# Optimization experiments

Measured on AMD Instinct MI355X. Metric: run time of the kernel, lower is better.

Reference implementation:

```python
import jax, jax.numpy as jnp
import numpy as np

DIM = 1024
CTX_DIM = 768
H = 16


def setup_inputs() -> dict:
    key = jax.random.key(0)
    k1, k2, k3, k4, k5 = jax.random.split(key, 5)
    x = jax.random.normal(k1, (2, 2048, DIM), dtype=jnp.float32)
    context = jax.random.normal(k2, (2, 2048, CTX_DIM), dtype=jnp.float32)
    # Linear weights stored as [in, out] (y = x @ W); no biases per module.
    s = 0.02
    Wq = jax.random.normal(k3, (DIM, DIM), dtype=jnp.float32) * s
    Wkv = jax.random.normal(k4, (CTX_DIM, 2 * DIM), dtype=jnp.float32) * s
    Wo = jax.random.normal(k5, (DIM, DIM), dtype=jnp.float32) * s
    return {"x": x, "context": context, "Wq": Wq, "Wkv": Wkv, "Wo": Wo}


def reference(x, context, Wq, Wkv, Wo):
    B, N, C = x.shape
    Dh = C // H  # head dim
    scale = Dh ** -0.5
    M = context.shape[1]
    q = (x @ Wq).reshape(B, N, H, Dh).transpose(0, 2, 1, 3)      # [B,H,N,Dh]
    kv = context @ Wkv                                            # [B,M,2C]
    k, v = jnp.split(kv, 2, axis=-1)
    k = k.reshape(B, M, H, Dh).transpose(0, 2, 1, 3)              # [B,H,M,Dh]
    v = v.reshape(B, M, H, Dh).transpose(0, 2, 1, 3)              # [B,H,M,Dh]
    attn = jax.nn.softmax(jnp.einsum('bhnd,bhmd->bhnm', q, k) * scale, axis=-1)
    out = jnp.einsum('bhnm,bhmd->bhnd', attn, v)                  # [B,H,N,Dh]
    out = out.transpose(0, 2, 1, 3).reshape(B, N, C)
    return out @ Wo  # dropout is identity in eval / p=0
```

## Files before the change

### kernel.cpp

```cpp
#include <hip/hip_runtime.h>

typedef __attribute__((ext_vector_type(4))) float f32x4;
typedef __attribute__((ext_vector_type(8))) short short8;
typedef __attribute__((ext_vector_type(4))) unsigned int u32x4;
typedef unsigned short u16;
typedef unsigned int u32;
typedef unsigned long long u64;

__device__ __forceinline__ u16 f2bf(float f) {
  u32 u = __builtin_bit_cast(u32, f);
  u += 0x7fffu + ((u >> 16) & 1u);
  return (u16)(u >> 16);
}
__device__ __forceinline__ u16 f2bf_t(float f) {
  return (u16)(__builtin_bit_cast(u32, f) >> 16);
}

__device__ __forceinline__ void gl2lds16(const u16* g, const u16* l) {
  __builtin_amdgcn_global_load_lds(
      (const __attribute__((address_space(1))) u32*)g,
      (__attribute__((address_space(3))) u32*)(u32)(u64)l,
      16, 0, 0);
}

__device__ __forceinline__ void cast_body(const float* __restrict__ s,
                                          u16* __restrict__ d, int blk,
                                          int tid) {
  long i = (long)blk * 256 + tid;
  const f32x4* sp = (const f32x4*)(s + i * 8);
  f32x4 a = sp[0], b = sp[1];
  u16 t[8];
#pragma unroll
  for (int j = 0; j < 4; j++) {
    t[j] = f2bf(a[j]);
    t[4 + j] = f2bf(b[j]);
  }
  *(u32x4*)(d + i * 8) = *(u32x4*)t;
}

__device__ __forceinline__ void transpose_body(const float* __restrict__ W,
                                               u16* __restrict__ WT, int K,
                                               int N, int k0, int n0, int tid,
                                               u16* T) {
#pragma unroll
  for (int i = 0; i < 4; i++) {
    int c = tid + 256 * i;
    int row = c >> 4;
    int ch = c & 15;
    f32x4 f = *(const f32x4*)(W + (long)(k0 + row) * N + n0 + ch * 4);
#pragma unroll
    for (int j = 0; j < 4; j++) T[(ch * 4 + j) * 72 + row] = f2bf(f[j]);
  }
  __syncthreads();
#pragma unroll
  for (int i = 0; i < 2; i++) {
    int c = tid + 256 * i;
    int row = c >> 3;
    int ch = c & 7;
    u32x4 v = *(u32x4*)&T[row * 72 + ch * 8];
    *(u32x4*)(WT + (long)(n0 + row) * K + k0 + ch * 8) = v;
  }
}

__global__ __launch_bounds__(256) void prep(
    const float* __restrict__ x, const float* __restrict__ ctx,
    const float* __restrict__ Wq, const float* __restrict__ Wkv,
    const float* __restrict__ Wo, u16* __restrict__ xb,
    u16* __restrict__ ctxb, u16* __restrict__ wqT, u16* __restrict__ wkvT,
    u16* __restrict__ woT) {
  __shared__ __align__(16) u16 T[64 * 72];
  const int b = blockIdx.x, tid = threadIdx.x;
  if (b < 2048) {
    cast_body(x, xb, b, tid);
  } else if (b < 3584) {
    cast_body(ctx, ctxb, b - 2048, tid);
  } else if (b < 3840) {
    int idx = b - 3584;
    transpose_body(Wq, wqT, 1024, 1024, (idx >> 4) * 64, (idx & 15) * 64, tid, T);
  } else if (b < 4224) {
    int idx = b - 3840;
    transpose_body(Wkv, wkvT, 768, 2048, (idx >> 5) * 64, (idx & 31) * 64, tid, T);
  } else {
    int idx = b - 4224;
    transpose_body(Wo, woT, 1024, 1024, (idx >> 4) * 64, (idx & 15) * 64, tid, T);
  }
}

__device__ __forceinline__ void gemm128_core(
    const u16* __restrict__ A, const u16* __restrict__ Bt, int Kstride,
    int Klen, long brow, long bcol, int tid, u16* As, u16* Bs,
    f32x4 (&acc)[4][4]) {
  const int lane = tid & 63, wv = tid >> 6;
  const int l15 = lane & 15, quad = lane >> 4;
  const int wr = (wv >> 1) * 64, wc = (wv & 1) * 64;
  const int sr = lane >> 3, sc = lane & 7;
  const int csw = ((sc ^ sr) & 7) * 8;

  const u16* ag[4];
  const u16* bg[4];
  const u16* al[4];
  const u16* bl[4];
#pragma unroll
  for (int n = 0; n < 4; n++) {
    int row = wv * 32 + n * 8;
    ag[n] = A + (brow + row + sr) * (long)Kstride + csw;
    al[n] = &As[row * 64];
    bg[n] = Bt + (bcol + row + sr) * (long)Kstride + csw;
    bl[n] = &Bs[row * 64];
  }

  for (int kt = 0; kt < Klen; kt += 64) {
    __syncthreads();
#pragma unroll
    for (int n = 0; n < 4; n++) gl2lds16(ag[n] + kt, al[n]);
#pragma unroll
    for (int n = 0; n < 4; n++) gl2lds16(bg[n] + kt, bl[n]);
    __syncthreads();
#pragma unroll
    for (int kk = 0; kk < 2; kk++) {
      short8 af[4], bf[4];
#pragma unroll
      for (int i = 0; i < 4; i++) {
        int row = wr + i * 16 + l15;
        af[i] = *(short8*)&As[row * 64 + (((kk * 4 + quad) ^ (row & 7)) << 3)];
      }
#pragma unroll
      for (int j = 0; j < 4; j++) {
        int row = wc + j * 16 + l15;
        bf[j] = *(short8*)&Bs[row * 64 + (((kk * 4 + quad) ^ (row & 7)) << 3)];
      }
#pragma unroll
      for (int i = 0; i < 4; i++)
#pragma unroll
        for (int j = 0; j < 4; j++)
          acc[i][j] = __builtin_amdgcn_mfma_f32_16x16x32_bf16(
              af[i], bf[j], acc[i][j], 0, 0, 0);
    }
  }
}

__global__ __launch_bounds__(256, 3) void fused_qkv(
    const u16* __restrict__ xb, const u16* __restrict__ ctxb,
    const u16* __restrict__ wqT, const u16* __restrict__ wkvT,
    u16* __restrict__ Qb, u16* __restrict__ Kfrag, u16* __restrict__ Vfrag,
    float qscale) {
  __shared__ __align__(16) u16 As[128 * 64];
  __shared__ __align__(16) u16 Bs[128 * 64];
  const int tid = threadIdx.x;
  const int lane = tid & 63, wv = tid >> 6;
  const int l15 = lane & 15, quad = lane >> 4;
  const int wr = (wv >> 1) * 64, wc = (wv & 1) * 64;

  f32x4 acc[4][4];
#pragma unroll
  for (int i = 0; i < 4; i++)
#pragma unroll
    for (int j = 0; j < 4; j++) acc[i][j] = (f32x4){0.f, 0.f, 0.f, 0.f};

  int bid = blockIdx.x;
  if (bid < 256) {
    long brow = (long)(bid >> 3) * 128, bcol = (long)(bid & 7) * 128;
    gemm128_core(xb, wqT, 1024, 1024, brow, bcol, tid, As, Bs, acc);
#pragma unroll
    for (int i = 0; i < 4; i++)
#pragma unroll
      for (int j = 0; j < 4; j++)
#pragma unroll
        for (int r = 0; r < 4; r++) {
          long row = brow + wr + i * 16 + quad * 4 + r;
          long col = bcol + wc + j * 16 + l15;
          Qb[row * 1024 + col] = f2bf(acc[i][j][r] * qscale);
        }
    return;
  }

  bid -= 256;
  long brow = (long)(bid >> 4) * 128, bcol = (long)(bid & 15) * 128;
  gemm128_core(ctxb, wkvT, 768, 768, brow, bcol, tid, As, Bs, acc);

  const bool is_k = (bcol < 1024);
  __syncthreads();
#pragma unroll
  for (int round = 0; round < 2; round++) {
    if ((wv >> 1) == round) {
      if (is_k) {
#pragma unroll
        for (int i = 0; i < 4; i++)
#pragma unroll
          for (int j = 0; j < 4; j++) {
            int d = j * 16 + l15;
            int off = (wv & 1) * 4096 + ((d >> 5) * 4 + i) * 512 +
                      (((d >> 3) & 3) * 16 + quad * 4) * 8 + (d & 7);
#pragma unroll
            for (int r = 0; r < 4; r++) As[off + r * 8] = f2bf(acc[i][j][r]);
          }
      } else {
#pragma unroll
        for (int i = 0; i < 4; i++)
#pragma unroll
          for (int j = 0; j < 4; j++) {
            int off = (wv & 1) * 4096 + ((i >> 1) * 4 + j) * 512 +
                      (quad * 16 + l15) * 8 + (i & 1) * 4;
            u16 t4[4];
#pragma unroll
            for (int r = 0; r < 4; r++) t4[r] = f2bf(acc[i][j][r]);
            *(u64*)&As[off] = *(const u64*)t4;
          }
      }
    }
    __syncthreads();
    long mg = brow + round * 64;
    int b_ = (int)(mg >> 11), mt = (int)((mg >> 6) & 31);
#pragma unroll
    for (int h2 = 0; h2 < 2; h2++) {
      int h = (int)((is_k ? bcol : bcol - 1024) >> 6) + h2;
      u16* dst = (is_k ? Kfrag : Vfrag) + ((long)(b_ * 16 + h) * 32 + mt) * 4096;
#pragma unroll
      for (int p = 0; p < 2; p++) {
        int c = p * 256 + tid;
        *(u32x4*)(dst + c * 8) = *(u32x4*)&As[h2 * 4096 + c * 8];
      }
    }
    __syncthreads();
  }
}

__global__ __launch_bounds__(256, 3) void gemm_o(
    const u16* __restrict__ A, const u16* __restrict__ Bt,
    float* __restrict__ C) {
  __shared__ __align__(16) u16 As[128 * 64];
  __shared__ __align__(16) u16 Bs[128 * 64];
  const int tid = threadIdx.x;
  const int lane = tid & 63, wv = tid >> 6;
  const int l15 = lane & 15, quad = lane >> 4;
  const int wr = (wv >> 1) * 64, wc = (wv & 1) * 64;
  long brow = (long)blockIdx.y * 128, bcol = (long)blockIdx.x * 128;

  f32x4 acc[4][4];
#pragma unroll
  for (int i = 0; i < 4; i++)
#pragma unroll
    for (int j = 0; j < 4; j++) acc[i][j] = (f32x4){0.f, 0.f, 0.f, 0.f};

  gemm128_core(A, Bt, 1024, 1024, brow, bcol, tid, As, Bs, acc);

#pragma unroll
  for (int i = 0; i < 4; i++)
#pragma unroll
    for (int j = 0; j < 4; j++)
#pragma unroll
      for (int r = 0; r < 4; r++) {
        long row = brow + wr + i * 16 + quad * 4 + r;
        long col = bcol + wc + j * 16 + l15;
        C[row * 1024 + col] = acc[i][j][r];
      }
}

__global__ __launch_bounds__(256, 2) void attn_kernel(
    const u16* __restrict__ Q, const u16* __restrict__ Kfrag,
    const u16* __restrict__ Vfrag, u16* __restrict__ AO) {
  const int tid = threadIdx.x;
  const int lane = tid & 63, wave = tid >> 6;
  const int l15 = lane & 15, quad = lane >> 4;
  const int bh = blockIdx.y;
  const int b = bh >> 4, h = bh & 15;
  const long qrow0 = (long)b * 2048 + blockIdx.x * 128;

  short8 qf[2][2];
#pragma unroll
  for (int qt = 0; qt < 2; qt++)
#pragma unroll
    for (int kk = 0; kk < 2; kk++)
      qf[qt][kk] = *(const short8*)&Q[(qrow0 + wave * 32 + qt * 16 + l15) * 1024 +
                                      h * 64 + kk * 32 + quad * 8];

  f32x4 O[2][5];
#pragma unroll
  for (int qt = 0; qt < 2; qt++)
#pragma unroll
    for (int dt = 0; dt < 5; dt++) O[qt][dt] = (f32x4){0.f, 0.f, 0.f, 0.f};

  u32x4 ones_u = {0x3F803F80u, 0x3F803F80u, 0x3F803F80u, 0x3F803F80u};
  short8 ones = __builtin_bit_cast(short8, ones_u);

  const u16* kbase = Kfrag + (long)bh * 32 * 4096 + lane * 8;
  const u16* vbase = Vfrag + (long)bh * 32 * 4096 + lane * 8;

  auto load_k = [&](short8(&kf)[2][4], int tile) {
    const u16* kt = kbase + (long)tile * 4096;
#pragma unroll
    for (int kk = 0; kk < 2; kk++)
#pragma unroll
      for (int t = 0; t < 4; t++)
        kf[kk][t] = *(const short8*)(kt + (kk * 4 + t) * 512);
  };

  auto step = [&](short8(&kc)[2][4], short8(&kn)[2][4], int tile) {
    short8 vf[2][4];
    const u16* vt = vbase + (long)tile * 4096;
#pragma unroll
    for (int kk = 0; kk < 2; kk++)
#pragma unroll
      for (int dt = 0; dt < 4; dt++)
        vf[kk][dt] = *(const short8*)(vt + (kk * 4 + dt) * 512);
    if (tile + 1 < 32) load_k(kn, tile + 1);

    f32x4 s[4][2];
#pragma unroll
    for (int m4 = 0; m4 < 4; m4++)
#pragma unroll
      for (int qt = 0; qt < 2; qt++) s[m4][qt] = (f32x4){0.f, 0.f, 0.f, 0.f};
#pragma unroll
    for (int kk = 0; kk < 2; kk++)
#pragma unroll
      for (int m4 = 0; m4 < 4; m4++)
#pragma unroll
        for (int qt = 0; qt < 2; qt++)
          s[m4][qt] = __builtin_amdgcn_mfma_f32_16x16x32_bf16(
              kc[kk][m4], qf[qt][kk], s[m4][qt], 0, 0, 0);

#pragma unroll
    for (int kk = 0; kk < 2; kk++) {
#pragma unroll
      for (int qt = 0; qt < 2; qt++) {
        u32 w[4];
#pragma unroll
        for (int half = 0; half < 2; half++) {
          f32x4 sv = s[2 * kk + half][qt];
          u32 lo = (u32)f2bf_t(__builtin_amdgcn_exp2f(sv[0] - 24.f)) |
                   ((u32)f2bf_t(__builtin_amdgcn_exp2f(sv[1] - 24.f)) << 16);
          u32 hi = (u32)f2bf_t(__builtin_amdgcn_exp2f(sv[2] - 24.f)) |
                   ((u32)f2bf_t(__builtin_amdgcn_exp2f(sv[3] - 24.f)) << 16);
          w[half * 2] = lo;
          w[half * 2 + 1] = hi;
        }
        short8 pa = __builtin_bit_cast(short8, *(u32x4*)w);
#pragma unroll
        for (int dt = 0; dt < 4; dt++)
          O[qt][dt] = __builtin_amdgcn_mfma_f32_16x16x32_bf16(
              pa, vf[kk][dt], O[qt][dt], 0, 0, 0);
        O[qt][4] = __builtin_amdgcn_mfma_f32_16x16x32_bf16(
            pa, ones, O[qt][4], 0, 0, 0);
      }
    }
  };

  short8 ka[2][4], kb2[2][4];
  load_k(ka, 0);
  for (int tile = 0; tile < 32; tile += 2) {
    step(ka, kb2, tile);
    step(kb2, ka, tile + 1);
  }

#pragma unroll
  for (int qt = 0; qt < 2; qt++) {
    float inv[4];
#pragma unroll
    for (int r = 0; r < 4; r++) inv[r] = 1.f / O[qt][4][r];
#pragma unroll
    for (int dt = 0; dt < 4; dt++)
#pragma unroll
      for (int r = 0; r < 4; r++) {
        long row = qrow0 + wave * 32 + qt * 16 + quad * 4 + r;
        int col = h * 64 + dt * 16 + l15;
        AO[row * 1024 + col] = f2bf(O[qt][dt][r] * inv[r]);
      }
  }
}

extern "C" void kernel_launch(void* const* d_in, const int* in_sizes, int n_in,
                              void* d_out, int out_size, void* d_ws,
                              size_t ws_size, hipStream_t stream) {
  const float* x = (const float*)d_in[0];
  const float* ctx = (const float*)d_in[1];
  const float* Wq = (const float*)d_in[2];
  const float* Wkv = (const float*)d_in[3];
  const float* Wo = (const float*)d_in[4];
  float* out = (float*)d_out;

  u16* ws = (u16*)d_ws;
  u16* wqT = ws;
  u16* wkvT = wqT + 1048576;
  u16* woT = wkvT + 1572864;
  u16* Qb = woT + 1048576;
  u16* Kfrag = Qb + 4194304;
  u16* Vfrag = Kfrag + 4194304;
  u16* xb = Vfrag + 4194304;
  u16* ctxb = xb + 4194304;
  u16* AOb = xb;

  const float qscale = 0.125f * 1.4426950408889634f;

  prep<<<dim3(4480), 256, 0, stream>>>(x, ctx, Wq, Wkv, Wo, xb, ctxb, wqT,
                                       wkvT, woT);

  fused_qkv<<<dim3(768), 256, 0, stream>>>(xb, ctxb, wqT, wkvT, Qb, Kfrag,
                                           Vfrag, qscale);

  attn_kernel<<<dim3(16, 32), 256, 0, stream>>>(Qb, Kfrag, Vfrag, AOb);

  gemm_o<<<dim3(8, 32), 256, 0, stream>>>(AOb, woT, out);
}
```

Measured before the change: 183.7 us.

## Pre-swizzle GEMM operands into MFMA fragment layout and stream from global

The prep kernel now writes x, context, the weights, and the attention output directly in per-lane MFMA fragment order. The GEMMs can then load operands straight from global memory into registers with double buffering, with no LDS staging and no barriers. This removes the LDS round-trip and per-k-tile syncs, at the cost of more register pressure (launch bounds drop to 2 waves per SIMD) and no cross-wave operand reuse through LDS, so redundant global/L2 traffic rises. Attention also flattens its grid and emits its output through an LDS staging tile.

```diff
diff --git a/kernel.cpp b/kernel.cpp
--- a/kernel.cpp
+++ b/kernel.cpp
@@ -16,32 +16,25 @@
   return (u16)(__builtin_bit_cast(u32, f) >> 16);
 }
 
-__device__ __forceinline__ void gl2lds16(const u16* g, const u16* l) {
-  __builtin_amdgcn_global_load_lds(
-      (const __attribute__((address_space(1))) u32*)g,
-      (__attribute__((address_space(3))) u32*)(u32)(u64)l,
-      16, 0, 0);
-}
-
-__device__ __forceinline__ void cast_body(const float* __restrict__ s,
-                                          u16* __restrict__ d, int blk,
-                                          int tid) {
-  long i = (long)blk * 256 + tid;
-  const f32x4* sp = (const f32x4*)(s + i * 8);
-  f32x4 a = sp[0], b = sp[1];
-  u16 t[8];
-#pragma unroll
-  for (int j = 0; j < 4; j++) {
-    t[j] = f2bf(a[j]);
-    t[4 + j] = f2bf(b[j]);
-  }
-  *(u32x4*)(d + i * 8) = *(u32x4*)t;
-}
-
-__device__ __forceinline__ void transpose_body(const float* __restrict__ W,
-                                               u16* __restrict__ WT, int K,
-                                               int N, int k0, int n0, int tid,
-                                               u16* T) {
+
+__device__ __forceinline__ void cast_stage(const float* __restrict__ src,
+                                           int stride, int m0, int k0, int tid,
+                                           u16* T) {
+  int row = tid >> 2, cg = tid & 3;
+  const float* p = src + (long)(m0 + row) * stride + k0 + cg * 16;
+  u16 tmp[16];
+#pragma unroll
+  for (int q = 0; q < 4; q++) {
+    f32x4 f = ((const f32x4*)p)[q];
+#pragma unroll
+    for (int j = 0; j < 4; j++) tmp[q * 4 + j] = f2bf(f[j]);
+  }
+  *(u32x4*)&T[row * 72 + cg * 16] = ((u32x4*)tmp)[0];
+  *(u32x4*)&T[row * 72 + cg * 16 + 8] = ((u32x4*)tmp)[1];
+}
+
+__device__ __forceinline__ void trans_stage(const float* __restrict__ W, int N,
+                                            int k0, int n0, int tid, u16* T) {
 #pragma unroll
   for (int i = 0; i < 4; i++) {
     int c = tid + 256 * i;
@@ -51,101 +44,110 @@
 #pragma unroll
     for (int j = 0; j < 4; j++) T[(ch * 4 + j) * 72 + row] = f2bf(f[j]);
   }
-  __syncthreads();
-#pragma unroll
-  for (int i = 0; i < 2; i++) {
-    int c = tid + 256 * i;
-    int row = c >> 3;
-    int ch = c & 7;
-    u32x4 v = *(u32x4*)&T[row * 72 + ch * 8];
-    *(u32x4*)(WT + (long)(n0 + row) * K + k0 + ch * 8) = v;
+}
+
+__device__ __forceinline__ void frag_emit(const u16* T, u16* __restrict__ out,
+                                          int r0t, int kt, int KT, int tid) {
+#pragma unroll
+  for (int p = 0; p < 2; p++) {
+    int s = tid + 256 * p;
+    int sub = s >> 7, kk = (s >> 6) & 1, lane = s & 63;
+    const u16* src = &T[(sub * 16 + (s & 15)) * 72 + kk * 32 + ((s >> 4) & 3) * 8];
+    u16* dst = out + (((long)(r0t + sub) * KT + kt) * 2 + kk) * 512 + lane * 8;
+    *(u32x4*)dst = *(const u32x4*)src;
   }
 }
 
 __global__ __launch_bounds__(256) void prep(
     const float* __restrict__ x, const float* __restrict__ ctx,
     const float* __restrict__ Wq, const float* __restrict__ Wkv,
-    const float* __restrict__ Wo, u16* __restrict__ xb,
-    u16* __restrict__ ctxb, u16* __restrict__ wqT, u16* __restrict__ wkvT,
-    u16* __restrict__ woT) {
+    const float* __restrict__ Wo, u16* __restrict__ xfrag,
+    u16* __restrict__ ctxfrag, u16* __restrict__ wqfrag,
+    u16* __restrict__ wkvfrag, u16* __restrict__ wofrag) {
   __shared__ __align__(16) u16 T[64 * 72];
-  const int b = blockIdx.x, tid = threadIdx.x;
-  if (b < 2048) {
-    cast_body(x, xb, b, tid);
-  } else if (b < 3584) {
-    cast_body(ctx, ctxb, b - 2048, tid);
-  } else if (b < 3840) {
-    int idx = b - 3584;
-    transpose_body(Wq, wqT, 1024, 1024, (idx >> 4) * 64, (idx & 15) * 64, tid, T);
-  } else if (b < 4224) {
-    int idx = b - 3840;
-    transpose_body(Wkv, wkvT, 768, 2048, (idx >> 5) * 64, (idx & 31) * 64, tid, T);
+  const int bid = blockIdx.x, tid = threadIdx.x;
+  const float* src;
+  u16* out;
+  int m0, k0, KT, stride;
+  bool isA;
+  if (bid < 1024) {
+    isA = true; src = x; out = xfrag; stride = 1024; KT = 16;
+    m0 = (bid >> 4) * 64; k0 = (bid & 15) * 64;
+  } else if (bid < 1792) {
+    int i = bid - 1024;
+    isA = true; src = ctx; out = ctxfrag; stride = 768; KT = 12;
+    m0 = (i / 12) * 64; k0 = (i % 12) * 64;
+  } else if (bid < 2048) {
+    int i = bid - 1792;
+    isA = false; src = Wq; out = wqfrag; stride = 1024; KT = 16;
+    k0 = (i >> 4) * 64; m0 = (i & 15) * 64;
+  } else if (bid < 2432) {
+    int i = bid - 2048;
+    isA = false; src = Wkv; out = wkvfrag; stride = 2048; KT = 12;
+    k0 = (i >> 5) * 64; m0 = (i & 31) * 64;
   } else {
-    int idx = b - 4224;
-    transpose_body(Wo, woT, 1024, 1024, (idx >> 4) * 64, (idx & 15) * 64, tid, T);
-  }
-}
-
-__device__ __forceinline__ void gemm128_core(
-    const u16* __restrict__ A, const u16* __restrict__ Bt, int Kstride,
-    int Klen, long brow, long bcol, int tid, u16* As, u16* Bs,
-    f32x4 (&acc)[4][4]) {
-  const int lane = tid & 63, wv = tid >> 6;
-  const int l15 = lane & 15, quad = lane >> 4;
-  const int wr = (wv >> 1) * 64, wc = (wv & 1) * 64;
-  const int sr = lane >> 3, sc = lane & 7;
-  const int csw = ((sc ^ sr) & 7) * 8;
-
-  const u16* ag[4];
-  const u16* bg[4];
-  const u16* al[4];
-  const u16* bl[4];
+    int i = bid - 2432;
+    isA = false; src = Wo; out = wofrag; stride = 1024; KT = 16;
+    k0 = (i >> 4) * 64; m0 = (i & 15) * 64;
+  }
+  if (isA)
+    cast_stage(src, stride, m0, k0, tid, T);
+  else
+    trans_stage(src, stride, k0, m0, tid, T);
+  __syncthreads();
+  frag_emit(T, out, m0 >> 4, k0 >> 6, KT, tid);
+}
+
+__device__ __forceinline__ void mfma_block(f32x4 (&acc)[4][4],
+                                           short8 (&af)[2][4],
+                                           short8 (&bf)[2][4]) {
+#pragma unroll
+  for (int kk = 0; kk < 2; kk++)
+#pragma unroll
+    for (int i = 0; i < 4; i++)
+#pragma unroll
+      for (int j = 0; j < 4; j++)
+        acc[i][j] = __builtin_amdgcn_mfma_f32_16x16x32_bf16(
+            af[kk][i], bf[kk][j], acc[i][j], 0, 0, 0);
+}
+
+template <int KT>
+__device__ __forceinline__ void gemm_stream(const u16* __restrict__ AF,
+                                            const u16* __restrict__ BF,
+                                            long rt0, long nt0, int lane,
+                                            int wv, f32x4 (&acc)[4][4]) {
+  const u16* ab[4];
+  const u16* bb[4];
 #pragma unroll
   for (int n = 0; n < 4; n++) {
-    int row = wv * 32 + n * 8;
-    ag[n] = A + (brow + row + sr) * (long)Kstride + csw;
-    al[n] = &As[row * 64];
-    bg[n] = Bt + (bcol + row + sr) * (long)Kstride + csw;
-    bl[n] = &Bs[row * 64];
-  }
-
-  for (int kt = 0; kt < Klen; kt += 64) {
-    __syncthreads();
-#pragma unroll
-    for (int n = 0; n < 4; n++) gl2lds16(ag[n] + kt, al[n]);
-#pragma unroll
-    for (int n = 0; n < 4; n++) gl2lds16(bg[n] + kt, bl[n]);
-    __syncthreads();
-#pragma unroll
-    for (int kk = 0; kk < 2; kk++) {
-      short8 af[4], bf[4];
-#pragma unroll
-      for (int i = 0; i < 4; i++) {
-        int row = wr + i * 16 + l15;
-        af[i] = *(short8*)&As[row * 64 + (((kk * 4 + quad) ^ (row & 7)) << 3)];
+    ab[n] = AF + ((rt0 + (wv >> 1) * 4 + n) * KT) * 1024 + lane * 8;
+    bb[n] = BF + ((nt0 + (wv & 1) * 4 + n) * KT) * 1024 + lane * 8;
+  }
+  short8 a0[2][4], b0[2][4], a1[2][4], b1[2][4];
+  auto ld = [&](short8(&A)[2][4], short8(&B)[2][4], int kt) {
+#pragma unroll
+    for (int kk = 0; kk < 2; kk++)
+#pragma unroll
+      for (int n = 0; n < 4; n++) {
+        A[kk][n] = *(const short8*)(ab[n] + kt * 1024 + kk * 512);
+        B[kk][n] = *(const short8*)(bb[n] + kt * 1024 + kk * 512);
       }
-#pragma unroll
-      for (int j = 0; j < 4; j++) {
-        int row = wc + j * 16 + l15;
-        bf[j] = *(short8*)&Bs[row * 64 + (((kk * 4 + quad) ^ (row & 7)) << 3)];
-      }
-#pragma unroll
-      for (int i = 0; i < 4; i++)
-#pragma unroll
-        for (int j = 0; j < 4; j++)
-          acc[i][j] = __builtin_amdgcn_mfma_f32_16x16x32_bf16(
-              af[i], bf[j], acc[i][j], 0, 0, 0);
-    }
-  }
-}
-
-__global__ __launch_bounds__(256, 3) void fused_qkv(
-    const u16* __restrict__ xb, const u16* __restrict__ ctxb,
-    const u16* __restrict__ wqT, const u16* __restrict__ wkvT,
+  };
+  ld(a0, b0, 0);
+  for (int kt = 0; kt < KT; kt += 2) {
+    if (kt + 1 < KT) ld(a1, b1, kt + 1);
+    mfma_block(acc, a0, b0);
+    if (kt + 2 < KT) ld(a0, b0, kt + 2);
+    mfma_block(acc, a1, b1);
+  }
+}
+
+__global__ __launch_bounds__(256, 2) void fused_qkv(
+    const u16* __restrict__ xfrag, const u16* __restrict__ ctxfrag,
+    const u16* __restrict__ wqfrag, const u16* __restrict__ wkvfrag,
     u16* __restrict__ Qb, u16* __restrict__ Kfrag, u16* __restrict__ Vfrag,
     float qscale) {
-  __shared__ __align__(16) u16 As[128 * 64];
-  __shared__ __align__(16) u16 Bs[128 * 64];
+  __shared__ __align__(16) u16 As[8192];
   const int tid = threadIdx.x;
   const int lane = tid & 63, wv = tid >> 6;
   const int l15 = lane & 15, quad = lane >> 4;
@@ -159,8 +161,9 @@
 
   int bid = blockIdx.x;
   if (bid < 256) {
-    long brow = (long)(bid >> 3) * 128, bcol = (long)(bid & 7) * 128;
-    gemm128_core(xb, wqT, 1024, 1024, brow, bcol, tid, As, Bs, acc);
+    long rt0 = (long)(bid >> 3) * 8, nt0 = (long)(bid & 7) * 8;
+    gemm_stream<16>(xfrag, wqfrag, rt0, nt0, lane, wv, acc);
+    long brow = rt0 * 16, bcol = nt0 * 16;
 #pragma unroll
     for (int i = 0; i < 4; i++)
 #pragma unroll
@@ -175,8 +178,9 @@
   }
 
   bid -= 256;
-  long brow = (long)(bid >> 4) * 128, bcol = (long)(bid & 15) * 128;
-  gemm128_core(ctxb, wkvT, 768, 768, brow, bcol, tid, As, Bs, acc);
+  long rt0 = (long)(bid >> 4) * 8, nt0 = (long)(bid & 15) * 8;
+  gemm_stream<12>(ctxfrag, wkvfrag, rt0, nt0, lane, wv, acc);
+  long brow = rt0 * 16, bcol = nt0 * 16;
 
   const bool is_k = (bcol < 1024);
   __syncthreads();
@@ -225,16 +229,14 @@
   }
 }
 
-__global__ __launch_bounds__(256, 3) void gemm_o(
-    const u16* __restrict__ A, const u16* __restrict__ Bt,
+__global__ __launch_bounds__(256, 2) void gemm_o(
+    const u16* __restrict__ AOF, const u16* __restrict__ wofrag,
     float* __restrict__ C) {
-  __shared__ __align__(16) u16 As[128 * 64];
-  __shared__ __align__(16) u16 Bs[128 * 64];
   const int tid = threadIdx.x;
   const int lane = tid & 63, wv = tid >> 6;
   const int l15 = lane & 15, quad = lane >> 4;
   const int wr = (wv >> 1) * 64, wc = (wv & 1) * 64;
-  long brow = (long)blockIdx.y * 128, bcol = (long)blockIdx.x * 128;
+  long rt0 = (long)(blockIdx.x >> 3) * 8, nt0 = (long)(blockIdx.x & 7) * 8;
 
   f32x4 acc[4][4];
 #pragma unroll
@@ -242,8 +244,9 @@
 #pragma unroll
     for (int j = 0; j < 4; j++) acc[i][j] = (f32x4){0.f, 0.f, 0.f, 0.f};
 
-  gemm128_core(A, Bt, 1024, 1024, brow, bcol, tid, As, Bs, acc);
-
+  gemm_stream<16>(AOF, wofrag, rt0, nt0, lane, wv, acc);
+
+  long brow = rt0 * 16, bcol = nt0 * 16;
 #pragma unroll
   for (int i = 0; i < 4; i++)
 #pragma unroll
@@ -258,13 +261,14 @@
 
 __global__ __launch_bounds__(256, 2) void attn_kernel(
     const u16* __restrict__ Q, const u16* __restrict__ Kfrag,
-    const u16* __restrict__ Vfrag, u16* __restrict__ AO) {
+    const u16* __restrict__ Vfrag, u16* __restrict__ AOF) {
+  __shared__ __align__(16) u16 T2[128 * 72];
   const int tid = threadIdx.x;
   const int lane = tid & 63, wave = tid >> 6;
   const int l15 = lane & 15, quad = lane >> 4;
-  const int bh = blockIdx.y;
+  const int bh = blockIdx.x & 31;
   const int b = bh >> 4, h = bh & 15;
-  const long qrow0 = (long)b * 2048 + blockIdx.x * 128;
+  const long qrow0 = (long)b * 2048 + (blockIdx.x >> 5) * 128;
 
   short8 qf[2][2];
 #pragma unroll
@@ -360,11 +364,19 @@
 #pragma unroll
     for (int dt = 0; dt < 4; dt++)
 #pragma unroll
-      for (int r = 0; r < 4; r++) {
-        long row = qrow0 + wave * 32 + qt * 16 + quad * 4 + r;
-        int col = h * 64 + dt * 16 + l15;
-        AO[row * 1024 + col] = f2bf(O[qt][dt][r] * inv[r]);
-      }
+      for (int r = 0; r < 4; r++)
+        T2[(wave * 32 + qt * 16 + quad * 4 + r) * 72 + dt * 16 + l15] =
+            f2bf(O[qt][dt][r] * inv[r]);
+  }
+  __syncthreads();
+  const long rtb = qrow0 >> 4;
+#pragma unroll
+  for (int p = 0; p < 4; p++) {
+    int s = tid + 256 * p;
+    int rt_l = s >> 7, kk = (s >> 6) & 1, ln = s & 63;
+    const u16* src = &T2[(rt_l * 16 + (s & 15)) * 72 + kk * 32 + ((s >> 4) & 3) * 8];
+    u16* dst = AOF + (((rtb + rt_l) * 16 + h) * 2 + kk) * 512 + ln * 8;
+    *(u32x4*)dst = *(const u32x4*)src;
   }
 }
 
@@ -379,25 +391,25 @@
   float* out = (float*)d_out;
 
   u16* ws = (u16*)d_ws;
-  u16* wqT = ws;
-  u16* wkvT = wqT + 1048576;
-  u16* woT = wkvT + 1572864;
-  u16* Qb = woT + 1048576;
+  u16* wqfrag = ws;
+  u16* wkvfrag = wqfrag + 1048576;
+  u16* wofrag = wkvfrag + 1572864;
+  u16* Qb = wofrag + 1048576;
   u16* Kfrag = Qb + 4194304;
   u16* Vfrag = Kfrag + 4194304;
-  u16* xb = Vfrag + 4194304;
-  u16* ctxb = xb + 4194304;
-  u16* AOb = xb;
+  u16* xfrag = Vfrag + 4194304;
+  u16* ctxfrag = xfrag + 4194304;
+  u16* AOF = xfrag;
 
   const float qscale = 0.125f * 1.4426950408889634f;
 
-  prep<<<dim3(4480), 256, 0, stream>>>(x, ctx, Wq, Wkv, Wo, xb, ctxb, wqT,
-                                       wkvT, woT);
-
-  fused_qkv<<<dim3(768), 256, 0, stream>>>(xb, ctxb, wqT, wkvT, Qb, Kfrag,
-                                           Vfrag, qscale);
-
-  attn_kernel<<<dim3(16, 32), 256, 0, stream>>>(Qb, Kfrag, Vfrag, AOb);
-
-  gemm_o<<<dim3(8, 32), 256, 0, stream>>>(AOb, woT, out);
-}
+  prep<<<dim3(2688), 256, 0, stream>>>(x, ctx, Wq, Wkv, Wo, xfrag, ctxfrag,
+                                       wqfrag, wkvfrag, wofrag);
+
+  fused_qkv<<<dim3(768), 256, 0, stream>>>(xfrag, ctxfrag, wqfrag, wkvfrag,
+                                           Qb, Kfrag, Vfrag, qscale);
+
+  attn_kernel<<<dim3(512), 256, 0, stream>>>(Qb, Kfrag, Vfrag, AOF);
+
+  gemm_o<<<dim3(256), 256, 0, stream>>>(AOF, wofrag, out);
+}
```

Measured after the change: 192.8 us. 5.0% more time.
